# Kernel optimization log

Hardware: AMD Instinct MI355X
Metric: run time of the kernel (lower is better)

## Reference

```python
import jax, jax.numpy as jnp
import numpy as np
from jax import lax

DN = ('NCDHW', 'OIDHW', 'NCDHW')
BN_EPS = 1e-5  # eval-mode BatchNorm3d with running_mean=0, running_var=1


def conv3d(x, w, b):
    y = lax.conv_general_dilated(x, w, window_strides=(1, 1, 1),
                                 padding=[(1, 1)] * 3, dimension_numbers=DN)
    return y + b[None, :, None, None, None]


def maxpool2(x):
    return lax.reduce_window(x, -jnp.inf, lax.max,
                             (1, 1, 2, 2, 2), (1, 1, 2, 2, 2), 'VALID')


def spline_block(x, cw, cb, knots, sw, w1, w2, g, beta):
    # SplineConv3d: conv -> (BSpline3D blend with SiLU) -> BN(eval) -> maxpool
    y = conv3d(x, cw, cb)                                   # [b,c,d,h,w]
    basis = jnp.maximum(y[..., None] - knots, 0.0) ** 3     # [b,c,d,h,w,k]
    sp = jnp.einsum('bcdhwk,ck->bcdhw', basis, sw)
    out = (w1[None, :, None, None, None] * sp
           + w2[None, :, None, None, None] * (y * jax.nn.sigmoid(y)))
    scale = (g / jnp.sqrt(1.0 + BN_EPS))[None, :, None, None, None]
    return maxpool2(out * scale + beta[None, :, None, None, None])


def setup_inputs() -> dict:
    key = jax.random.key(0)
    ks = iter(jax.random.split(key, 40))
    def nrm(shape, s=1.0):
        return jax.random.normal(next(ks), shape, dtype=jnp.float32) * s
    d = {}
    d['x'] = nrm((2, 1, 64, 64, 64))
    for cin, cout, t in [(1, 32, '1'), (32, 64, '2'), (64, 128, '3')]:
        d[f'c{t}_w'] = nrm((cout, cin, 3, 3, 3), 0.1)
        d[f'c{t}_b'] = nrm((cout,), 0.01)
        d[f'c{t}_knots'] = jnp.linspace(-1.0, 1.0, 10).astype(jnp.float32)
        d[f'c{t}_sw'] = nrm((cout, 10), 0.2)
        d[f'c{t}_w1'] = nrm((cout,), 0.2)
        d[f'c{t}_w2'] = nrm((cout,), 0.2)
        d[f'bn{t}_g'] = 1.0 + nrm((cout,), 0.1)
        d[f'bn{t}_b'] = nrm((cout,), 0.1)
    d['fc1_w'] = nrm((256, 128), 0.05)
    d['fc1_b'] = nrm((256,), 0.01)
    d['fc2_w'] = nrm((2, 256), 0.05)
    d['fc2_b'] = nrm((2,), 0.01)
    return d


def reference(x,
              c1_w, c1_b, c1_knots, c1_sw, c1_w1, c1_w2, bn1_g, bn1_b,
              c2_w, c2_b, c2_knots, c2_sw, c2_w1, c2_w2, bn2_g, bn2_b,
              c3_w, c3_b, c3_knots, c3_sw, c3_w1, c3_w2, bn3_g, bn3_b,
              fc1_w, fc1_b, fc2_w, fc2_b):
    h = spline_block(x, c1_w, c1_b, c1_knots, c1_sw, c1_w1, c1_w2, bn1_g, bn1_b)
    h = spline_block(h, c2_w, c2_b, c2_knots, c2_sw, c2_w1, c2_w2, bn2_g, bn2_b)
    h = spline_block(h, c3_w, c3_b, c3_knots, c3_sw, c3_w1, c3_w2, bn3_g, bn3_b)
    h = h.mean(axis=(2, 3, 4))          # AdaptiveAvgPool3d((1,1,1)) + flatten
    h = jax.nn.relu(h @ fc1_w.T + fc1_b)  # dropout is identity in eval mode
    return h @ fc2_w.T + fc2_b
```

## Files before the change

### kernel.cpp

```cpp
#include <hip/hip_runtime.h>
#include <math.h>


#define GLOBAL_AS __attribute__((address_space(1)))
#define LDS_AS    __attribute__((address_space(3)))

static __device__ __forceinline__ void async_ld16(const float* g, float* l) {
    __builtin_amdgcn_global_load_lds((const GLOBAL_AS void*)g, (LDS_AS void*)l,
                                     16, 0, 0);
}

__global__ __launch_bounds__(256) void repack_kernel(
    const float* __restrict__ w1, const float* __restrict__ w2,
    const float* __restrict__ w3,
    float* __restrict__ o1, float* __restrict__ o2, float* __restrict__ o3,
    float* __restrict__ zbuf, float* __restrict__ pooled)
{
    const int i = blockIdx.x * 256 + threadIdx.x;
    const float* src;
    float* dst;
    if (i < 32)            { src = w1 + i * 27;           dst = o1 + i * 28; }
    else if (i < 2080)     { const int j = i - 32;   src = w2 + j * 27; dst = o2 + j * 28; }
    else if (i < 10272)    { const int j = i - 2080; src = w3 + j * 27; dst = o3 + j * 28; }
    else {
        if (i < 10288) zbuf[i - 10272] = 0.0f;
        else if (i < 10544) pooled[i - 10288] = 0.0f;
        return;
    }
#pragma unroll
    for (int t = 0; t < 27; t++) dst[t] = src[t];
    dst[27] = 0.0f;
}

template <int TPB_, int CIN, int CSPLIT, int G,
          int WDT, int WHT, int WWT, int BD, int BH, int BW, bool FMEAN>
__global__ __launch_bounds__(TPB_, 2) void spline_block_kernel(
    const float* __restrict__ x,
    const float4* __restrict__ wpk,
    const float* __restrict__ cb,
    const float* __restrict__ knots,
    const float* __restrict__ sw,
    const float* __restrict__ w1,
    const float* __restrict__ w2,
    const float* __restrict__ g,
    const float* __restrict__ beta,
    const float* __restrict__ zbuf,
    float* __restrict__ out,
    int N, int Cout, int D, int H, int W,
    int ntiles, int nthw, int ntw)
{
    constexpr int NSW    = BD * BH * BW;
    constexpr int NW     = TPB_ / 64;
    constexpr int CPG    = CIN / CSPLIT;
    constexpr int ID     = 2 * WDT + 2;
    constexpr int IH     = 2 * WHT + 2;
    constexpr int CHK    = (WWT + 4) / 2;
    constexpr int PITCH  = CHK * 4;
    constexpr int ROWS   = ID * IH;
    constexpr int CHUNKS = ROWS * CHK;
    constexpr int PHYS   = CHUNKS * 4;
    constexpr int NCH    = (CHUNKS + 63) / 64;
    constexpr int BUFS   = (CPG > 1) ? 2 : 1;
    static_assert(NW == NSW * CSPLIT, "waves = spatial-tiles x cin-split");
    static_assert(WDT * WHT * WWT == 64, "one wave per spatial tile");
    static_assert(CIN % CSPLIT == 0, "cin divisible");
    static_assert(G == 4, "acc layout assumes G==4");
    static_assert(NCH <= 32, "mask fits u32");
    static_assert(NCH == 6, "s_waitcnt vmcnt(6) literal assumes 6 issues/cin");
    static_assert(CSPLIT == 1 ||
                  (CSPLIT - 1) * NSW * 64 * G * 8 <= NW * BUFS * PHYS,
                  "reduction scratch fits in tile");

    __shared__ __align__(16) float tile[NW][BUFS][PHYS];
    __shared__ float4 stbl[G * 11];

    const int PD = D >> 1, PH = H >> 1, PW = W >> 1;
    const int groups = Cout / G;
    const int tid  = threadIdx.x;
    const int wv   = tid >> 6;
    const int lane = tid & 63;
    const int sw_  = wv % NSW;
    const int cg   = wv / NSW;

    const int bx      = blockIdx.x;
    const int tile_id = bx % ntiles;
    const int t1      = bx / ntiles;
    const int grp     = t1 % groups;
    const int n       = t1 / groups;
    const int c0      = grp * G;
    const int cinbase = cg * CPG;
    const int cinbase_u = __builtin_amdgcn_readfirstlane(cinbase);

    const int td  = tile_id / nthw;
    const int rem = tile_id % nthw;
    const int th_ = rem / ntw;
    const int tw_ = rem % ntw;

    for (int i = tid; i < G * 11; i += TPB_) {
        const int gg  = i / 11;
        const int cnt = i % 11;
        const int c   = c0 + gg;
        float A = 0.f, B3 = 0.f, C3 = 0.f, Dd = 0.f;
        for (int j = 0; j < cnt; j++) {
            const float s = sw[c * 10 + j];
            const float k = knots[j];
            A  += s;
            B3 += 3.0f * s * k;
            C3 += 3.0f * s * k * k;
            Dd += s * k * k * k;
        }
        stbl[i] = make_float4(A, B3, C3, Dd);
    }

    const int swd = sw_ / (BH * BW);
    const int r2  = sw_ % (BH * BW);
    const int swh = r2 / BW;
    const int sww = r2 % BW;
    const int pd0 = td  * (BD * WDT) + swd * WDT;
    const int ph0 = th_ * (BH * WHT) + swh * WHT;
    const int pw0 = tw_ * (BW * WWT) + sww * WWT;

    const int pwl = lane % WWT;
    const int phl = (lane / WWT) % WHT;
    const int pdl = lane / (WWT * WHT);

    const int d0 = 2 * pd0 - 1, h0 = 2 * ph0 - 1;
    const int w0 = 2 * pw0 - 1;
    const int wb = w0 & ~3;
    const int woff = w0 - wb;

    int off[NCH];
    unsigned vm = 0;
#pragma unroll
    for (int k = 0; k < NCH; k++) {
        const int chunk = lane + 64 * k;
        const int row = chunk / CHK, cs = chunk - row * CHK;
        const int dz = row / IH, hy = row - dz * IH;
        const int dd = d0 + dz, hh = h0 + hy;
        const int wsd = wb + cs * 4;
        const bool ok = (chunk < CHUNKS) &
                        ((unsigned)dd < (unsigned)D) &
                        ((unsigned)hh < (unsigned)H) &
                        ((unsigned)wsd < (unsigned)W);
        off[k] = ok ? (dd * H + hh) * W + wsd : 0;
        vm |= (unsigned)ok << k;
    }

    const size_t chstride = (size_t)D * H * W;
    const float* xn = x + (size_t)n * CIN * chstride;

    float acc[G][8];
#pragma unroll
    for (int gg = 0; gg < G; gg++)
#pragma unroll
        for (int i = 0; i < 8; i++) acc[gg][i] = 0.0f;

    __syncthreads();

    auto stage = [&](int ci, int buf) {
        const float* xc = xn + (size_t)ci * chstride;
        float* dst = &tile[wv][buf][0];
#pragma unroll
        for (int k = 0; k < NCH; k++) {
            const int chunk = lane + 64 * k;
            if ((k + 1) * 64 <= CHUNKS || chunk < CHUNKS) {
                const float* src = ((vm >> k) & 1) ? (xc + off[k]) : zbuf;
                async_ld16(src, dst + chunk * 4);
            }
        }
    };

    stage(cinbase, 0);

#pragma unroll 1
    for (int s = 0; s < CPG; s++) {
        const int cur = s & (BUFS - 1);
        if (s + 1 < CPG) {
            stage(cinbase + s + 1, cur ^ 1);
            asm volatile("s_waitcnt vmcnt(6)" ::: "memory");
        } else {
            asm volatile("s_waitcnt vmcnt(0)" ::: "memory");
        }

        const int ci_u = cinbase_u + s;
        const float* tb = &tile[wv][cur][0];
        float r[64];
#pragma unroll
        for (int dz = 0; dz < 4; dz++)
#pragma unroll
        for (int dy = 0; dy < 4; dy++) {
            const int rb = ((2 * pdl + dz) * IH + (2 * phl + dy)) * PITCH +
                           woff + 2 * pwl;
            r[(dz * 4 + dy) * 4 + 0] = tb[rb + 0];
            r[(dz * 4 + dy) * 4 + 1] = tb[rb + 1];
            r[(dz * 4 + dy) * 4 + 2] = tb[rb + 2];
            r[(dz * 4 + dy) * 4 + 3] = tb[rb + 3];
        }

#pragma unroll
        for (int gg = 0; gg < G; gg++) {
            const float4* wq = wpk + ((size_t)(c0 + gg) * CIN + ci_u) * 7;
            float4 q[7];
#pragma unroll
            for (int ch = 0; ch < 7; ch++) q[ch] = wq[ch];
#pragma unroll
            for (int ch = 0; ch < 7; ch++) {
#pragma unroll
                for (int j = 0; j < 4; j++) {
                    const int tap = ch * 4 + j;
                    if (tap < 27) {
                        const float wvj = (j == 0) ? q[ch].x : (j == 1) ? q[ch].y
                                        : (j == 2) ? q[ch].z : q[ch].w;
                        const int kd = tap / 9, kh = (tap % 9) / 3, kw = tap % 3;
#pragma unroll
                        for (int od = 0; od < 2; od++)
#pragma unroll
                        for (int oh = 0; oh < 2; oh++)
#pragma unroll
                        for (int ow = 0; ow < 2; ow++)
                            acc[gg][(od * 2 + oh) * 2 + ow] =
                                fmaf(wvj,
                                     r[((od + kd) * 4 + (oh + kh)) * 4 + (ow + kw)],
                                     acc[gg][(od * 2 + oh) * 2 + ow]);
                    }
                }
            }
        }
    }

    float* af = &acc[0][0];
    if (CSPLIT > 1) {
        __syncthreads();
        float* scratch = &tile[0][0][0];
        if (cg > 0) {
#pragma unroll
            for (int idx = 0; idx < G * 8; idx++)
                scratch[((idx * (CSPLIT - 1) + (cg - 1)) * NSW + sw_) * 64 + lane]
                    = af[idx];
        }
        __syncthreads();
        if (cg == 0) {
#pragma unroll
            for (int idx = 0; idx < G * 8; idx++) {
                float s2 = af[idx];
                for (int j = 0; j < CSPLIT - 1; j++)
                    s2 += scratch[((idx * (CSPLIT - 1) + j) * NSW + sw_) * 64 + lane];
                af[idx] = s2;
            }
        }
    }

    if (cg == 0) {
        const int pdg = pd0 + pdl, phg = ph0 + phl, pwg = pw0 + pwl;
        const float inv_vol = 1.0f / (float)(PD * PH * PW);
#pragma unroll
        for (int gg = 0; gg < G; gg++) {
            const int c = c0 + gg;
            const float bias = cb[c];
            const float W1 = w1[c], W2 = w2[c];
            const float scale = g[c] * rsqrtf(1.0f + 1e-5f);
            const float bb = beta[c];
            float m = -INFINITY;
#pragma unroll
            for (int i = 0; i < 8; i++) {
                const float y = acc[gg][i] + bias;
                int idx = (int)floorf((y + 1.0f) * 4.5f) + 1;
                idx = min(max(idx, 0), 10);
                const float4 cf = stbl[gg * 11 + idx];
                const float sp = ((cf.x * y - cf.y) * y + cf.z) * y - cf.w;
                const float silu = y / (1.0f + __expf(-y));
                const float o = fmaf(W1 * sp + W2 * silu, scale, bb);
                m = fmaxf(m, o);
            }
            if constexpr (FMEAN) {
                float ssum = m;
#pragma unroll
                for (int o2 = 32; o2 > 0; o2 >>= 1)
                    ssum += __shfl_down(ssum, o2, 64);
                if (lane == 0)
                    atomicAdd(&out[(size_t)n * Cout + c], ssum * inv_vol);
            } else {
                out[((size_t)(n * Cout + c) * PD + pdg) * PH * PW +
                    phg * PW + pwg] = m;
            }
        }
    }
}

__global__ __launch_bounds__(256) void fc_kernel(
    const float* __restrict__ pooled,
    const float* __restrict__ w1, const float* __restrict__ b1,
    const float* __restrict__ w2, const float* __restrict__ b2,
    float* __restrict__ out)
{
    __shared__ float hbuf[2][256];
    const int j = threadIdx.x;
#pragma unroll
    for (int nn = 0; nn < 2; nn++) {
        float s = b1[j];
        for (int k = 0; k < 128; k++)
            s = fmaf(pooled[nn * 128 + k], w1[j * 128 + k], s);
        hbuf[nn][j] = fmaxf(s, 0.0f);
    }
    __syncthreads();
    const int wid = j >> 6, lane = j & 63;
    const int nn = wid >> 1, oo = wid & 1;
    float s = 0.0f;
    for (int k = lane; k < 256; k += 64) s += hbuf[nn][k] * w2[oo * 256 + k];
#pragma unroll
    for (int off = 32; off > 0; off >>= 1) s += __shfl_down(s, off, 64);
    if (lane == 0) out[nn * 2 + oo] = s + b2[oo];
}

extern "C" void kernel_launch(void* const* d_in, const int* in_sizes, int n_in,
                              void* d_out, int out_size, void* d_ws, size_t ws_size,
                              hipStream_t stream) {
    const float* x      = (const float*)d_in[0];
    const float* c1_w   = (const float*)d_in[1];
    const float* c1_b   = (const float*)d_in[2];
    const float* c1_kn  = (const float*)d_in[3];
    const float* c1_sw  = (const float*)d_in[4];
    const float* c1_w1  = (const float*)d_in[5];
    const float* c1_w2  = (const float*)d_in[6];
    const float* bn1_g  = (const float*)d_in[7];
    const float* bn1_b  = (const float*)d_in[8];
    const float* c2_w   = (const float*)d_in[9];
    const float* c2_b   = (const float*)d_in[10];
    const float* c2_kn  = (const float*)d_in[11];
    const float* c2_sw  = (const float*)d_in[12];
    const float* c2_w1  = (const float*)d_in[13];
    const float* c2_w2  = (const float*)d_in[14];
    const float* bn2_g  = (const float*)d_in[15];
    const float* bn2_b  = (const float*)d_in[16];
    const float* c3_w   = (const float*)d_in[17];
    const float* c3_b   = (const float*)d_in[18];
    const float* c3_kn  = (const float*)d_in[19];
    const float* c3_sw  = (const float*)d_in[20];
    const float* c3_w1  = (const float*)d_in[21];
    const float* c3_w2  = (const float*)d_in[22];
    const float* bn3_g  = (const float*)d_in[23];
    const float* bn3_b  = (const float*)d_in[24];
    const float* fc1_w  = (const float*)d_in[25];
    const float* fc1_b  = (const float*)d_in[26];
    const float* fc2_w  = (const float*)d_in[27];
    const float* fc2_b  = (const float*)d_in[28];

    float* ws = (float*)d_ws;
    float* h1     = ws;
    float* h2     = h1 + 2097152;
    float* pooled = h2 + 524288;
    float* zbuf   = pooled + 256;
    float* wp1    = zbuf + 16;
    float* wp2    = wp1 + 896;
    float* wp3    = wp2 + 57344;

    repack_kernel<<<dim3(42), dim3(256), 0, stream>>>(c1_w, c2_w, c3_w,
                                                      wp1, wp2, wp3, zbuf, pooled);

    spline_block_kernel<256, 1, 1, 4, 2, 4, 8, 2, 2, 1, false>
        <<<dim3(2048), dim3(256), 0, stream>>>(
        x, (const float4*)wp1, c1_b, c1_kn, c1_sw, c1_w1, c1_w2, bn1_g, bn1_b,
        zbuf, h1, 2, 32, 64, 64, 64, 128, 16, 4);
    spline_block_kernel<256, 32, 2, 4, 2, 4, 8, 1, 1, 2, false>
        <<<dim3(1024), dim3(256), 0, stream>>>(
        h1, (const float4*)wp2, c2_b, c2_kn, c2_sw, c2_w1, c2_w2, bn2_g, bn2_b,
        zbuf, h2, 2, 64, 32, 32, 32, 32, 4, 1);
    spline_block_kernel<256, 64, 4, 4, 2, 4, 8, 1, 1, 1, true>
        <<<dim3(512), dim3(256), 0, stream>>>(
        h2, (const float4*)wp3, c3_b, c3_kn, c3_sw, c3_w1, c3_w2, bn3_g, bn3_b,
        zbuf, pooled, 2, 128, 16, 16, 16, 8, 2, 1);
    fc_kernel<<<dim3(1), dim3(256), 0, stream>>>(pooled, fc1_w, fc1_b, fc2_w, fc2_b,
                                                 (float*)d_out);
}
```

Measured before the change: 320.6 us.

## Fuse FC head into last spline block and widen channel group for block two

The separate FC kernel launch is removed. The last block of the third spline kernel, found through an atomic completion counter, now runs both FC layers using LDS scratch. Block two switches from 4 to 8 output channels per block, which halves its grid so each input tile load serves more channels. The G==8 setting depends on hidden accumulator-layout code that was only asserted for G==4. It also raises register pressure and may lower occupancy.

```diff
diff --git a/kernel.cpp b/kernel.cpp
--- a/kernel.cpp
+++ b/kernel.cpp
@@ -14,7 +14,8 @@
     const float* __restrict__ w1, const float* __restrict__ w2,
     const float* __restrict__ w3,
     float* __restrict__ o1, float* __restrict__ o2, float* __restrict__ o3,
-    float* __restrict__ zbuf, float* __restrict__ pooled)
+    float* __restrict__ zbuf, float* __restrict__ pooled,
+    float* __restrict__ cntf)
 {
     const int i = blockIdx.x * 256 + threadIdx.x;
     const float* src;
@@ -25,6 +26,7 @@
     else {
         if (i < 10288) zbuf[i - 10272] = 0.0f;
         else if (i < 10544) pooled[i - 10288] = 0.0f;
+        else if (i < 10560) cntf[i - 10544] = 0.0f;
         return;
     }
 #pragma unroll
@@ -46,6 +48,9 @@
     const float* __restrict__ beta,
     const float* __restrict__ zbuf,
     float* __restrict__ out,
+    const float* __restrict__ fw1, const float* __restrict__ fb1,
+    const float* __restrict__ fw2, const float* __restrict__ fb2,
+    float* __restrict__ dout, int* __restrict__ cnt,
     int N, int Cout, int D, int H, int W,
     int ntiles, int nthw, int ntw)
 {
@@ -64,15 +69,17 @@
     static_assert(NW == NSW * CSPLIT, "waves = spatial-tiles x cin-split");
     static_assert(WDT * WHT * WWT == 64, "one wave per spatial tile");
     static_assert(CIN % CSPLIT == 0, "cin divisible");
-    static_assert(G == 4, "acc layout assumes G==4");
+    static_assert(G == 4 || G == 8, "acc layout assumes G in {4,8}");
     static_assert(NCH <= 32, "mask fits u32");
     static_assert(NCH == 6, "s_waitcnt vmcnt(6) literal assumes 6 issues/cin");
     static_assert(CSPLIT == 1 ||
                   (CSPLIT - 1) * NSW * 64 * G * 8 <= NW * BUFS * PHYS,
                   "reduction scratch fits in tile");
+    static_assert(!FMEAN || TPB_ == 256, "fused fc assumes 256 threads");
 
     __shared__ __align__(16) float tile[NW][BUFS][PHYS];
     __shared__ float4 stbl[G * 11];
+    __shared__ int lastblk;
 
     const int PD = D >> 1, PH = H >> 1, PW = W >> 1;
     const int groups = Cout / G;
@@ -98,10 +105,10 @@
 
     for (int i = tid; i < G * 11; i += TPB_) {
         const int gg  = i / 11;
-        const int cnt = i % 11;
+        const int cnt2 = i % 11;
         const int c   = c0 + gg;
         float A = 0.f, B3 = 0.f, C3 = 0.f, Dd = 0.f;
-        for (int j = 0; j < cnt; j++) {
+        for (int j = 0; j < cnt2; j++) {
             const float s = sw[c * 10 + j];
             const float k = knots[j];
             A  += s;
@@ -285,31 +292,37 @@
             }
         }
     }
-}
-
-__global__ __launch_bounds__(256) void fc_kernel(
-    const float* __restrict__ pooled,
-    const float* __restrict__ w1, const float* __restrict__ b1,
-    const float* __restrict__ w2, const float* __restrict__ b2,
-    float* __restrict__ out)
-{
-    __shared__ float hbuf[2][256];
-    const int j = threadIdx.x;
-#pragma unroll
-    for (int nn = 0; nn < 2; nn++) {
-        float s = b1[j];
-        for (int k = 0; k < 128; k++)
-            s = fmaf(pooled[nn * 128 + k], w1[j * 128 + k], s);
-        hbuf[nn][j] = fmaxf(s, 0.0f);
-    }
-    __syncthreads();
-    const int wid = j >> 6, lane = j & 63;
-    const int nn = wid >> 1, oo = wid & 1;
-    float s = 0.0f;
-    for (int k = lane; k < 256; k += 64) s += hbuf[nn][k] * w2[oo * 256 + k];
-#pragma unroll
-    for (int off = 32; off > 0; off >>= 1) s += __shfl_down(s, off, 64);
-    if (lane == 0) out[nn * 2 + oo] = s + b2[oo];
+
+    if constexpr (FMEAN) {
+        __syncthreads();
+        if (tid == 0) {
+            __threadfence();
+            lastblk = (atomicAdd(cnt, 1) == (int)gridDim.x - 1);
+        }
+        __syncthreads();
+        if (lastblk) {
+            __threadfence();
+            float* fl = &tile[0][0][0];
+            fl[tid] = atomicAdd(&out[tid], 0.0f);
+            __syncthreads();
+#pragma unroll
+            for (int nn = 0; nn < 2; nn++) {
+                float s = fb1[tid];
+                for (int k = 0; k < 128; k++)
+                    s = fmaf(fl[nn * 128 + k], fw1[tid * 128 + k], s);
+                fl[256 + nn * 256 + tid] = fmaxf(s, 0.0f);
+            }
+            __syncthreads();
+            const int wid = tid >> 6, l2 = tid & 63;
+            const int nn = wid >> 1, oo = wid & 1;
+            float s = 0.0f;
+            for (int k = l2; k < 256; k += 64)
+                s += fl[256 + nn * 256 + k] * fw2[oo * 256 + k];
+#pragma unroll
+            for (int o2 = 32; o2 > 0; o2 >>= 1) s += __shfl_down(s, o2, 64);
+            if (l2 == 0) dout[nn * 2 + oo] = s + fb2[oo];
+        }
+    }
 }
 
 extern "C" void kernel_launch(void* const* d_in, const int* in_sizes, int n_in,
@@ -350,25 +363,27 @@
     float* h2     = h1 + 2097152;
     float* pooled = h2 + 524288;
     float* zbuf   = pooled + 256;
-    float* wp1    = zbuf + 16;
+    float* cntf   = zbuf + 16;
+    float* wp1    = cntf + 16;
     float* wp2    = wp1 + 896;
     float* wp3    = wp2 + 57344;
 
-    repack_kernel<<<dim3(42), dim3(256), 0, stream>>>(c1_w, c2_w, c3_w,
-                                                      wp1, wp2, wp3, zbuf, pooled);
+    repack_kernel<<<dim3(42), dim3(256), 0, stream>>>(
+        c1_w, c2_w, c3_w, wp1, wp2, wp3, zbuf, pooled, cntf);
 
     spline_block_kernel<256, 1, 1, 4, 2, 4, 8, 2, 2, 1, false>
         <<<dim3(2048), dim3(256), 0, stream>>>(
         x, (const float4*)wp1, c1_b, c1_kn, c1_sw, c1_w1, c1_w2, bn1_g, bn1_b,
-        zbuf, h1, 2, 32, 64, 64, 64, 128, 16, 4);
-    spline_block_kernel<256, 32, 2, 4, 2, 4, 8, 1, 1, 2, false>
-        <<<dim3(1024), dim3(256), 0, stream>>>(
+        zbuf, h1, nullptr, nullptr, nullptr, nullptr, nullptr, nullptr,
+        2, 32, 64, 64, 64, 128, 16, 4);
+    spline_block_kernel<256, 32, 2, 8, 2, 4, 8, 1, 1, 2, false>
+        <<<dim3(512), dim3(256), 0, stream>>>(
         h1, (const float4*)wp2, c2_b, c2_kn, c2_sw, c2_w1, c2_w2, bn2_g, bn2_b,
-        zbuf, h2, 2, 64, 32, 32, 32, 32, 4, 1);
+        zbuf, h2, nullptr, nullptr, nullptr, nullptr, nullptr, nullptr,
+        2, 64, 32, 32, 32, 32, 4, 1);
     spline_block_kernel<256, 64, 4, 4, 2, 4, 8, 1, 1, 1, true>
         <<<dim3(512), dim3(256), 0, stream>>>(
         h2, (const float4*)wp3, c3_b, c3_kn, c3_sw, c3_w1, c3_w2, bn3_g, bn3_b,
-        zbuf, pooled, 2, 128, 16, 16, 16, 8, 2, 1);
-    fc_kernel<<<dim3(1), dim3(256), 0, stream>>>(pooled, fc1_w, fc1_b, fc2_w, fc2_b,
-                                                 (float*)d_out);
+        zbuf, pooled, fc1_w, fc1_b, fc2_w, fc2_b, (float*)d_out, (int*)cntf,
+        2, 128, 16, 16, 16, 8, 2, 1);
 }
```

Measured after the change: 318.5 us. About the same (-0.7%).
